# Kernel optimization log

Hardware: AMD Instinct MI355X
Metric: run time of the kernel (lower is better)

## Reference

```python
import jax, jax.numpy as jnp
import numpy as np

N_NODES = 100000
N_EDGES = 1600000
IN_C, HID_C, OUT_C = 128, 128, 64


def gcn_conv(x, src, dst, n_nodes, W, b):
    # PyG GCNConv (normalize=True, add_self_loops=True):
    # out = D^{-1/2} (A+I) D^{-1/2} (x @ W^T) + b
    h = x @ W.T                                   # [N, out]
    deg = jax.ops.segment_sum(jnp.ones(src.shape, x.dtype), dst,
                              num_segments=n_nodes)  # includes self-loops
    dinv = jnp.where(deg > 0, jax.lax.rsqrt(deg), 0.0)
    norm = dinv[src] * dinv[dst]                  # [E+N]
    msg = h[src] * norm[:, None]                  # gather + scale
    out = jax.ops.segment_sum(msg, dst, num_segments=n_nodes)
    return out + b


def setup_inputs() -> dict:
    key = jax.random.key(0)
    ks = jax.random.split(key, 8)
    x = jax.random.normal(ks[0], (N_NODES, IN_C), dtype=jnp.float32)
    edge_index = jax.random.randint(ks[1], (2, N_EDGES), 0, N_NODES, dtype=jnp.int64)

    def lin(k, fan_out, fan_in):
        s = 1.0 / np.sqrt(fan_in)
        kw, kb = jax.random.split(k)
        W = jax.random.uniform(kw, (fan_out, fan_in), jnp.float32, -s, s)
        b = jax.random.uniform(kb, (fan_out,), jnp.float32, -s, s)
        return W, b

    W1, b1 = lin(ks[2], HID_C, IN_C)
    W2, b2 = lin(ks[3], HID_C, HID_C)
    W3, b3 = lin(ks[4], OUT_C, HID_C)
    return {"x": x, "edge_index": edge_index,
            "W1": W1, "b1": b1, "W2": W2, "b2": b2, "W3": W3, "b3": b3}


def reference(x, edge_index, W1, b1, W2, b2, W3, b3):
    n = x.shape[0]
    loop = jnp.arange(n, dtype=edge_index.dtype)
    src = jnp.concatenate([edge_index[0], loop])  # add self-loops once; identical per layer
    dst = jnp.concatenate([edge_index[1], loop])
    h = gcn_conv(x, src, dst, n, W1, b1)
    h = jax.nn.relu(h)
    h = gcn_conv(h, src, dst, n, W2, b2)
    h = jax.nn.relu(h)
    h = gcn_conv(h, src, dst, n, W3, b3)
    return h
```

## Files before the change

### kernel.cpp

```cpp
#include <hip/hip_runtime.h>


#define NPB 256
#define CAP 4672
#define BIN_WGS 128

typedef short bfrag __attribute__((ext_vector_type(8)));
typedef float f32x4 __attribute__((ext_vector_type(4)));
typedef unsigned short u16x8 __attribute__((ext_vector_type(8)));

__global__ __launch_bounds__(256) void init_cur(int* __restrict__ cur, int B) {
  int i = blockIdx.x * 256 + threadIdx.x;
  if (i < B) cur[i] = i * CAP;
}

__global__ __launch_bounds__(256) void bin_edges(const int* __restrict__ src,
                                                 const int* __restrict__ dst,
                                                 int* __restrict__ cur,
                                                 int* __restrict__ binned,
                                                 int E, int B) {
  __shared__ int lc[512];
  __shared__ int lbase[512];
  const int t = threadIdx.x;
  const int chunk = (E + BIN_WGS - 1) / BIN_WGS;
  const int e0 = blockIdx.x * chunk;
  const int e1 = min(E, e0 + chunk);

  for (int i = t; i < B; i += 256) lc[i] = 0;
  __syncthreads();
  for (int e = e0 + t; e < e1; e += 256) {
    int d = dst[e];
    atomicAdd(&lc[d >> 8], 1);
  }
  __syncthreads();
  for (int i = t; i < B; i += 256) {
    int c = lc[i];
    lbase[i] = c ? atomicAdd(&cur[i], c) : 0;
    lc[i] = 0;
  }
  __syncthreads();
  for (int e = e0 + t; e < e1; e += 256) {
    int d = dst[e];
    int s = __builtin_nontemporal_load(&src[e]);
    int bk = d >> 8;
    int p = lbase[bk] + atomicAdd(&lc[bk], 1);
    if (p < (bk + 1) * CAP)
      binned[p] = ((d & 255) << 24) | s;
  }
}

__global__ __launch_bounds__(256) void build_buckets(const int* __restrict__ binned,
                                                     const int* __restrict__ cur,
                                                     int* __restrict__ cols,
                                                     int2* __restrict__ off2,
                                                     float* __restrict__ dinv,
                                                     int N) {
  __shared__ int eb[CAP];
  __shared__ int ob[CAP];
  __shared__ int lc[256];
  __shared__ int sc[256];
  const int b = blockIdx.x;
  const int t = threadIdx.x;
  const int base = b * CAP;
  const int cntb = min(cur[b] - base, CAP);

  for (int i = t; i < cntb; i += 256) eb[i] = binned[base + i];
  lc[t] = 0;
  __syncthreads();
  for (int i = t; i < cntb; i += 256)
    atomicAdd(&lc[(unsigned)eb[i] >> 24], 1);
  __syncthreads();
  int myc = lc[t];
  sc[t] = myc;
  __syncthreads();
  for (int d = 1; d < 256; d <<= 1) {
    int a = (t >= d) ? sc[t - d] : 0;
    __syncthreads();
    sc[t] += a;
    __syncthreads();
  }
  int excl = sc[t] - myc;
  int node = b * NPB + t;
  if (node < N) {
    off2[node] = make_int2(base + excl, base + excl + myc);
    dinv[node] = rsqrtf((float)(myc + 1));
  }
  lc[t] = excl;
  __syncthreads();
  for (int i = t; i < cntb; i += 256) {
    int e = eb[i];
    int p = atomicAdd(&lc[(unsigned)e >> 24], 1);
    ob[p] = e & 0xFFFFFF;
  }
  __syncthreads();
  for (int i = t; i < cntb; i += 256) cols[base + i] = ob[i];
}

__device__ inline unsigned short bf16rne(float x) {
  unsigned u = __float_as_uint(x);
  return (unsigned short)((u + 0x7FFFu + ((u >> 16) & 1u)) >> 16);
}
__device__ inline float bf16lo(unsigned q) { return __uint_as_float(q << 16); }
__device__ inline float bf16hi(unsigned q) { return __uint_as_float(q & 0xFFFF0000u); }

#define LDP 136
template <int OUTC>
__global__ __launch_bounds__(256) void gemm_xw_mfma(const float* __restrict__ X,
                                                    const float* __restrict__ W,
                                                    const float* __restrict__ dinv,
                                                    unsigned short* __restrict__ Y,
                                                    int M) {
  __shared__ unsigned short Xhi[64 * LDP], Xlo[64 * LDP];
  __shared__ unsigned short Whi[64 * LDP], Wlo[64 * LDP];
  const int tid = threadIdx.x;
  const int m_base = blockIdx.x * 64;

  for (int idx = tid; idx < 64 * 16; idx += 256) {
    int r = idx >> 4, g = idx & 15;
    int m = m_base + r;
    float4 v0 = make_float4(0.f, 0.f, 0.f, 0.f), v1 = v0;
    if (m < M) {
      const float4* px = (const float4*)(X + (size_t)m * 128 + g * 8);
      v0 = px[0];
      v1 = px[1];
    }
    float vv[8] = {v0.x, v0.y, v0.z, v0.w, v1.x, v1.y, v1.z, v1.w};
    u16x8 hv, lv;
#pragma unroll
    for (int j = 0; j < 8; ++j) {
      unsigned short h = bf16rne(vv[j]);
      float res = vv[j] - __uint_as_float((unsigned)h << 16);
      hv[j] = h;
      lv[j] = bf16rne(res);
    }
    *(u16x8*)(Xhi + r * LDP + g * 8) = hv;
    *(u16x8*)(Xlo + r * LDP + g * 8) = lv;
  }

  const int lane = tid & 63;
  const int wv = tid >> 6;
  const int col_l = lane & 15;
  const int quad = lane >> 4;
  const int aBase = (wv * 16 + col_l) * LDP + quad * 8;
  const int bBase = col_l * LDP + quad * 8;

  for (int cc = 0; cc < OUTC; cc += 64) {
    __syncthreads();
    for (int idx = tid; idx < 64 * 16; idx += 256) {
      int r = idx >> 4, g = idx & 15;
      const float4* pw = (const float4*)(W + (size_t)(cc + r) * 128 + g * 8);
      float4 v0 = pw[0], v1 = pw[1];
      float vv[8] = {v0.x, v0.y, v0.z, v0.w, v1.x, v1.y, v1.z, v1.w};
      u16x8 hv, lv;
#pragma unroll
      for (int j = 0; j < 8; ++j) {
        unsigned short h = bf16rne(vv[j]);
        float res = vv[j] - __uint_as_float((unsigned)h << 16);
        hv[j] = h;
        lv[j] = bf16rne(res);
      }
      *(u16x8*)(Whi + r * LDP + g * 8) = hv;
      *(u16x8*)(Wlo + r * LDP + g * 8) = lv;
    }
    __syncthreads();

    f32x4 acc[4] = {{0.f, 0.f, 0.f, 0.f},
                    {0.f, 0.f, 0.f, 0.f},
                    {0.f, 0.f, 0.f, 0.f},
                    {0.f, 0.f, 0.f, 0.f}};
#pragma unroll
    for (int ks = 0; ks < 4; ++ks) {
      int ao = aBase + ks * 32;
      bfrag aHi = *(const bfrag*)(Xhi + ao);
      bfrag aLo = *(const bfrag*)(Xlo + ao);
#pragma unroll
      for (int t = 0; t < 4; ++t) {
        int bo = bBase + t * 16 * LDP + ks * 32;
        bfrag bHi = *(const bfrag*)(Whi + bo);
        bfrag bLo = *(const bfrag*)(Wlo + bo);
        acc[t] = __builtin_amdgcn_mfma_f32_16x16x32_bf16(aHi, bHi, acc[t], 0, 0, 0);
        acc[t] = __builtin_amdgcn_mfma_f32_16x16x32_bf16(aLo, bHi, acc[t], 0, 0, 0);
        acc[t] = __builtin_amdgcn_mfma_f32_16x16x32_bf16(aHi, bLo, acc[t], 0, 0, 0);
      }
    }

#pragma unroll
    for (int r = 0; r < 4; ++r) {
      int row = m_base + wv * 16 + quad * 4 + r;
      if (row < M) {
        float s = dinv[row];
#pragma unroll
        for (int t = 0; t < 4; ++t) {
          unsigned short h = bf16rne(acc[t][r] * s);
          Y[(size_t)row * OUTC + cc + t * 16 + col_l] = h;
        }
      }
    }
  }
}

template <int C, bool RELU>
__global__ __launch_bounds__(256) void aggregate(const void* __restrict__ xsv,
                                                 const int2* __restrict__ off2,
                                                 const int* __restrict__ cols,
                                                 const float* __restrict__ dinv,
                                                 const float* __restrict__ bias,
                                                 float* __restrict__ out, int N) {
  constexpr int V = C / 64;
  int wid = (int)((blockIdx.x * blockDim.x + threadIdx.x) >> 6);
  int lane = threadIdx.x & 63;
  if (wid >= N) return;

  float a0, a1 = 0.f;
  if constexpr (V == 2) {
    const unsigned* xs = (const unsigned*)xsv;
    unsigned q = xs[(size_t)wid * 64 + lane];
    a0 = bf16lo(q);
    a1 = bf16hi(q);
  } else {
    const unsigned short* xs = (const unsigned short*)xsv;
    a0 = __uint_as_float((unsigned)xs[(size_t)wid * 64 + lane] << 16);
  }

  int2 oo = off2[wid];
  int ebase = oo.x;
  int e1 = oo.y;
  while (ebase < e1) {
    int cnt = e1 - ebase;
    if (cnt > 64) cnt = 64;
    int col = (lane < cnt) ? __builtin_nontemporal_load(&cols[ebase + lane]) : 0;
    int j = 0;
    for (; j + 4 <= cnt; j += 4) {
      int s0 = __shfl(col, j), s1 = __shfl(col, j + 1);
      int s2 = __shfl(col, j + 2), s3 = __shfl(col, j + 3);
      if constexpr (V == 2) {
        const unsigned* xs = (const unsigned*)xsv;
        unsigned q0 = xs[(size_t)s0 * 64 + lane];
        unsigned q1 = xs[(size_t)s1 * 64 + lane];
        unsigned q2 = xs[(size_t)s2 * 64 + lane];
        unsigned q3 = xs[(size_t)s3 * 64 + lane];
        a0 += (bf16lo(q0) + bf16lo(q1)) + (bf16lo(q2) + bf16lo(q3));
        a1 += (bf16hi(q0) + bf16hi(q1)) + (bf16hi(q2) + bf16hi(q3));
      } else {
        const unsigned short* xs = (const unsigned short*)xsv;
        float t0 = __uint_as_float((unsigned)xs[(size_t)s0 * 64 + lane] << 16);
        float t1 = __uint_as_float((unsigned)xs[(size_t)s1 * 64 + lane] << 16);
        float t2 = __uint_as_float((unsigned)xs[(size_t)s2 * 64 + lane] << 16);
        float t3 = __uint_as_float((unsigned)xs[(size_t)s3 * 64 + lane] << 16);
        a0 += (t0 + t1) + (t2 + t3);
      }
    }
    for (; j < cnt; ++j) {
      int s = __shfl(col, j);
      if constexpr (V == 2) {
        const unsigned* xs = (const unsigned*)xsv;
        unsigned q = xs[(size_t)s * 64 + lane];
        a0 += bf16lo(q);
        a1 += bf16hi(q);
      } else {
        const unsigned short* xs = (const unsigned short*)xsv;
        a0 += __uint_as_float((unsigned)xs[(size_t)s * 64 + lane] << 16);
      }
    }
    ebase += cnt;
  }

  float dd = dinv[wid];
  if constexpr (V == 2) {
    float o0 = a0 * dd + bias[lane * 2];
    float o1 = a1 * dd + bias[lane * 2 + 1];
    if (RELU) {
      o0 = fmaxf(o0, 0.f);
      o1 = fmaxf(o1, 0.f);
    }
    __builtin_nontemporal_store(o0, &out[(size_t)wid * C + lane * 2]);
    __builtin_nontemporal_store(o1, &out[(size_t)wid * C + lane * 2 + 1]);
  } else {
    float o0 = a0 * dd + bias[lane];
    if (RELU) o0 = fmaxf(o0, 0.f);
    __builtin_nontemporal_store(o0, &out[(size_t)wid * C + lane]);
  }
}


extern "C" void kernel_launch(void* const* d_in, const int* in_sizes, int n_in,
                              void* d_out, int out_size, void* d_ws, size_t ws_size,
                              hipStream_t stream) {
  const float* x  = (const float*)d_in[0];
  const int*   ei = (const int*)d_in[1];
  const float* W1 = (const float*)d_in[2];
  const float* b1 = (const float*)d_in[3];
  const float* W2 = (const float*)d_in[4];
  const float* b2 = (const float*)d_in[5];
  const float* W3 = (const float*)d_in[6];
  const float* b3 = (const float*)d_in[7];

  const int N = in_sizes[0] / 128;
  const int E = in_sizes[1] / 2;
  const int* src = ei;
  const int* dst = ei + E;
  const int B = (N + NPB - 1) / NPB;

  char* w = (char*)d_ws;
  size_t p = 0;
  auto alloc = [&](size_t bytes) -> void* {
    void* r = w + p;
    p = (p + bytes + 255) & ~(size_t)255;
    return r;
  };
  float*    dinv   = (float*)alloc((size_t)N * 4);
  int2*     off2   = (int2*)alloc((size_t)N * 8);
  int*      cur    = (int*)alloc((size_t)B * 4);
  int*      binned = (int*)alloc((size_t)B * CAP * 4);
  int*      cols   = (int*)alloc((size_t)B * CAP * 4);
  unsigned short* xsb = (unsigned short*)alloc((size_t)N * 128 * 2);
  float*    bufB   = (float*)alloc((size_t)N * 128 * 4);

  init_cur<<<(B + 255) / 256, 256, 0, stream>>>(cur, B);
  bin_edges<<<BIN_WGS, 256, 0, stream>>>(src, dst, cur, binned, E, B);
  build_buckets<<<B, 256, 0, stream>>>(binned, cur, cols, off2, dinv, N);

  const int gb = (N + 63) / 64;
  const int ab = (N + 3) / 4;

  gemm_xw_mfma<128><<<gb, 256, 0, stream>>>(x, W1, dinv, xsb, N);
  aggregate<128, true><<<ab, 256, 0, stream>>>(xsb, off2, cols, dinv, b1, bufB, N);
  gemm_xw_mfma<128><<<gb, 256, 0, stream>>>(bufB, W2, dinv, xsb, N);
  aggregate<128, true><<<ab, 256, 0, stream>>>(xsb, off2, cols, dinv, b2, bufB, N);
  gemm_xw_mfma<64><<<gb, 256, 0, stream>>>(bufB, W3, dinv, xsb, N);
  aggregate<64, false><<<ab, 256, 0, stream>>>(xsb, off2, cols, dinv, b3,
                                               (float*)d_out, N);
}
```

Measured before the change: 459.5 us.

## Use 16-byte gathers over multiple edges per wave in aggregation; presplit weights

The aggregation kernel now has each lane load 8 bf16 channels (16 bytes) per neighbor, so a 64-lane wave covers several edges at once. Partial sums are then reduced across edge groups with xor-shuffles, and the output is written as vector stores. This targets the many small 4-byte gathers and the serial per-edge loop of the old kernel, at the cost of a cross-lane reduction and some masked wasted loads. Separately, the weight hi/lo bf16 split moves into a small pre-kernel, so each GEMM block no longer recomputes it.

```diff
diff --git a/kernel.cpp b/kernel.cpp
--- a/kernel.cpp
+++ b/kernel.cpp
@@ -103,10 +103,24 @@
 __device__ inline float bf16lo(unsigned q) { return __uint_as_float(q << 16); }
 __device__ inline float bf16hi(unsigned q) { return __uint_as_float(q & 0xFFFF0000u); }
 
+__global__ __launch_bounds__(256) void split_w(const float* __restrict__ W,
+                                               unsigned short* __restrict__ hi,
+                                               unsigned short* __restrict__ lo,
+                                               int total) {
+  int i = blockIdx.x * 256 + threadIdx.x;
+  if (i < total) {
+    float v = W[i];
+    unsigned short h = bf16rne(v);
+    hi[i] = h;
+    lo[i] = bf16rne(v - __uint_as_float((unsigned)h << 16));
+  }
+}
+
 #define LDP 136
 template <int OUTC>
 __global__ __launch_bounds__(256) void gemm_xw_mfma(const float* __restrict__ X,
-                                                    const float* __restrict__ W,
+                                                    const unsigned short* __restrict__ Whg,
+                                                    const unsigned short* __restrict__ Wlg,
                                                     const float* __restrict__ dinv,
                                                     unsigned short* __restrict__ Y,
                                                     int M) {
@@ -148,17 +162,8 @@
     __syncthreads();
     for (int idx = tid; idx < 64 * 16; idx += 256) {
       int r = idx >> 4, g = idx & 15;
-      const float4* pw = (const float4*)(W + (size_t)(cc + r) * 128 + g * 8);
-      float4 v0 = pw[0], v1 = pw[1];
-      float vv[8] = {v0.x, v0.y, v0.z, v0.w, v1.x, v1.y, v1.z, v1.w};
-      u16x8 hv, lv;
-#pragma unroll
-      for (int j = 0; j < 8; ++j) {
-        unsigned short h = bf16rne(vv[j]);
-        float res = vv[j] - __uint_as_float((unsigned)h << 16);
-        hv[j] = h;
-        lv[j] = bf16rne(res);
-      }
+      u16x8 hv = *(const u16x8*)(Whg + (size_t)(cc + r) * 128 + g * 8);
+      u16x8 lv = *(const u16x8*)(Wlg + (size_t)(cc + r) * 128 + g * 8);
       *(u16x8*)(Whi + r * LDP + g * 8) = hv;
       *(u16x8*)(Wlo + r * LDP + g * 8) = lv;
     }
@@ -200,85 +205,99 @@
 }
 
 template <int C, bool RELU>
-__global__ __launch_bounds__(256) void aggregate(const void* __restrict__ xsv,
-                                                 const int2* __restrict__ off2,
-                                                 const int* __restrict__ cols,
-                                                 const float* __restrict__ dinv,
-                                                 const float* __restrict__ bias,
-                                                 float* __restrict__ out, int N) {
-  constexpr int V = C / 64;
+__global__ __launch_bounds__(256) void aggregate2(const unsigned short* __restrict__ xs,
+                                                  const int2* __restrict__ off2,
+                                                  const int* __restrict__ cols,
+                                                  const float* __restrict__ dinv,
+                                                  const float* __restrict__ bias,
+                                                  float* __restrict__ out, int N) {
+  constexpr int CG = C / 8;
+  constexpr int EG = 64 / CG;
   int wid = (int)((blockIdx.x * blockDim.x + threadIdx.x) >> 6);
   int lane = threadIdx.x & 63;
   if (wid >= N) return;
-
-  float a0, a1 = 0.f;
-  if constexpr (V == 2) {
-    const unsigned* xs = (const unsigned*)xsv;
-    unsigned q = xs[(size_t)wid * 64 + lane];
-    a0 = bf16lo(q);
-    a1 = bf16hi(q);
-  } else {
-    const unsigned short* xs = (const unsigned short*)xsv;
-    a0 = __uint_as_float((unsigned)xs[(size_t)wid * 64 + lane] << 16);
+  const int eg = lane / CG;
+  const int cg = lane % CG;
+
+  float acc[8] = {0.f, 0.f, 0.f, 0.f, 0.f, 0.f, 0.f, 0.f};
+  if (eg == 0) {
+    uint4 d = *(const uint4*)(xs + (size_t)wid * C + cg * 8);
+    acc[0] = bf16lo(d.x); acc[1] = bf16hi(d.x);
+    acc[2] = bf16lo(d.y); acc[3] = bf16hi(d.y);
+    acc[4] = bf16lo(d.z); acc[5] = bf16hi(d.z);
+    acc[6] = bf16lo(d.w); acc[7] = bf16hi(d.w);
   }
 
   int2 oo = off2[wid];
   int ebase = oo.x;
-  int e1 = oo.y;
-  while (ebase < e1) {
-    int cnt = e1 - ebase;
+  const int eend = oo.y;
+  while (ebase < eend) {
+    int cnt = eend - ebase;
     if (cnt > 64) cnt = 64;
     int col = (lane < cnt) ? __builtin_nontemporal_load(&cols[ebase + lane]) : 0;
-    int j = 0;
-    for (; j + 4 <= cnt; j += 4) {
-      int s0 = __shfl(col, j), s1 = __shfl(col, j + 1);
-      int s2 = __shfl(col, j + 2), s3 = __shfl(col, j + 3);
-      if constexpr (V == 2) {
-        const unsigned* xs = (const unsigned*)xsv;
-        unsigned q0 = xs[(size_t)s0 * 64 + lane];
-        unsigned q1 = xs[(size_t)s1 * 64 + lane];
-        unsigned q2 = xs[(size_t)s2 * 64 + lane];
-        unsigned q3 = xs[(size_t)s3 * 64 + lane];
-        a0 += (bf16lo(q0) + bf16lo(q1)) + (bf16lo(q2) + bf16lo(q3));
-        a1 += (bf16hi(q0) + bf16hi(q1)) + (bf16hi(q2) + bf16hi(q3));
-      } else {
-        const unsigned short* xs = (const unsigned short*)xsv;
-        float t0 = __uint_as_float((unsigned)xs[(size_t)s0 * 64 + lane] << 16);
-        float t1 = __uint_as_float((unsigned)xs[(size_t)s1 * 64 + lane] << 16);
-        float t2 = __uint_as_float((unsigned)xs[(size_t)s2 * 64 + lane] << 16);
-        float t3 = __uint_as_float((unsigned)xs[(size_t)s3 * 64 + lane] << 16);
-        a0 += (t0 + t1) + (t2 + t3);
-      }
-    }
-    for (; j < cnt; ++j) {
-      int s = __shfl(col, j);
-      if constexpr (V == 2) {
-        const unsigned* xs = (const unsigned*)xsv;
-        unsigned q = xs[(size_t)s * 64 + lane];
-        a0 += bf16lo(q);
-        a1 += bf16hi(q);
-      } else {
-        const unsigned short* xs = (const unsigned short*)xsv;
-        a0 += __uint_as_float((unsigned)xs[(size_t)s * 64 + lane] << 16);
+    const int c1 = cnt - 1;
+    for (int j = 0; j < cnt; j += 4 * EG) {
+      int i0 = j + eg, i1 = i0 + EG, i2 = i1 + EG, i3 = i2 + EG;
+      int s0 = __shfl(col, min(i0, c1));
+      int s1 = __shfl(col, min(i1, c1));
+      int s2 = __shfl(col, min(i2, c1));
+      int s3 = __shfl(col, min(i3, c1));
+      uint4 d0 = *(const uint4*)(xs + (size_t)s0 * C + cg * 8);
+      uint4 d1 = *(const uint4*)(xs + (size_t)s1 * C + cg * 8);
+      uint4 d2 = *(const uint4*)(xs + (size_t)s2 * C + cg * 8);
+      uint4 d3 = *(const uint4*)(xs + (size_t)s3 * C + cg * 8);
+      if (i0 < cnt) {
+        acc[0] += bf16lo(d0.x); acc[1] += bf16hi(d0.x);
+        acc[2] += bf16lo(d0.y); acc[3] += bf16hi(d0.y);
+        acc[4] += bf16lo(d0.z); acc[5] += bf16hi(d0.z);
+        acc[6] += bf16lo(d0.w); acc[7] += bf16hi(d0.w);
+      }
+      if (i1 < cnt) {
+        acc[0] += bf16lo(d1.x); acc[1] += bf16hi(d1.x);
+        acc[2] += bf16lo(d1.y); acc[3] += bf16hi(d1.y);
+        acc[4] += bf16lo(d1.z); acc[5] += bf16hi(d1.z);
+        acc[6] += bf16lo(d1.w); acc[7] += bf16hi(d1.w);
+      }
+      if (i2 < cnt) {
+        acc[0] += bf16lo(d2.x); acc[1] += bf16hi(d2.x);
+        acc[2] += bf16lo(d2.y); acc[3] += bf16hi(d2.y);
+        acc[4] += bf16lo(d2.z); acc[5] += bf16hi(d2.z);
+        acc[6] += bf16lo(d2.w); acc[7] += bf16hi(d2.w);
+      }
+      if (i3 < cnt) {
+        acc[0] += bf16lo(d3.x); acc[1] += bf16hi(d3.x);
+        acc[2] += bf16lo(d3.y); acc[3] += bf16hi(d3.y);
+        acc[4] += bf16lo(d3.z); acc[5] += bf16hi(d3.z);
+        acc[6] += bf16lo(d3.w); acc[7] += bf16hi(d3.w);
       }
     }
     ebase += cnt;
   }
 
-  float dd = dinv[wid];
-  if constexpr (V == 2) {
-    float o0 = a0 * dd + bias[lane * 2];
-    float o1 = a1 * dd + bias[lane * 2 + 1];
+#pragma unroll
+  for (int m = CG; m < 64; m <<= 1) {
+#pragma unroll
+    for (int q = 0; q < 8; ++q) acc[q] += __shfl_xor(acc[q], m);
+  }
+
+  if (eg == 0) {
+    float dd = dinv[wid];
+    const float4 bA = *(const float4*)(bias + cg * 8);
+    const float4 bB = *(const float4*)(bias + cg * 8 + 4);
+    f32x4 oA, oB;
+    oA[0] = acc[0] * dd + bA.x; oA[1] = acc[1] * dd + bA.y;
+    oA[2] = acc[2] * dd + bA.z; oA[3] = acc[3] * dd + bA.w;
+    oB[0] = acc[4] * dd + bB.x; oB[1] = acc[5] * dd + bB.y;
+    oB[2] = acc[6] * dd + bB.z; oB[3] = acc[7] * dd + bB.w;
     if (RELU) {
-      o0 = fmaxf(o0, 0.f);
-      o1 = fmaxf(o1, 0.f);
-    }
-    __builtin_nontemporal_store(o0, &out[(size_t)wid * C + lane * 2]);
-    __builtin_nontemporal_store(o1, &out[(size_t)wid * C + lane * 2 + 1]);
-  } else {
-    float o0 = a0 * dd + bias[lane];
-    if (RELU) o0 = fmaxf(o0, 0.f);
-    __builtin_nontemporal_store(o0, &out[(size_t)wid * C + lane]);
+#pragma unroll
+      for (int q = 0; q < 4; ++q) {
+        oA[q] = fmaxf(oA[q], 0.f);
+        oB[q] = fmaxf(oB[q], 0.f);
+      }
+    }
+    __builtin_nontemporal_store(oA, (f32x4*)(out + (size_t)wid * C + cg * 8));
+    __builtin_nontemporal_store(oB, (f32x4*)(out + (size_t)wid * C + cg * 8 + 4));
   }
 }
 
@@ -315,19 +334,28 @@
   int*      cols   = (int*)alloc((size_t)B * CAP * 4);
   unsigned short* xsb = (unsigned short*)alloc((size_t)N * 128 * 2);
   float*    bufB   = (float*)alloc((size_t)N * 128 * 4);
+  unsigned short* w1h = (unsigned short*)alloc(128 * 128 * 2);
+  unsigned short* w1l = (unsigned short*)alloc(128 * 128 * 2);
+  unsigned short* w2h = (unsigned short*)alloc(128 * 128 * 2);
+  unsigned short* w2l = (unsigned short*)alloc(128 * 128 * 2);
+  unsigned short* w3h = (unsigned short*)alloc(64 * 128 * 2);
+  unsigned short* w3l = (unsigned short*)alloc(64 * 128 * 2);
 
   init_cur<<<(B + 255) / 256, 256, 0, stream>>>(cur, B);
   bin_edges<<<BIN_WGS, 256, 0, stream>>>(src, dst, cur, binned, E, B);
+  split_w<<<64, 256, 0, stream>>>(W1, w1h, w1l, 128 * 128);
+  split_w<<<64, 256, 0, stream>>>(W2, w2h, w2l, 128 * 128);
+  split_w<<<32, 256, 0, stream>>>(W3, w3h, w3l, 64 * 128);
   build_buckets<<<B, 256, 0, stream>>>(binned, cur, cols, off2, dinv, N);
 
   const int gb = (N + 63) / 64;
   const int ab = (N + 3) / 4;
 
-  gemm_xw_mfma<128><<<gb, 256, 0, stream>>>(x, W1, dinv, xsb, N);
-  aggregate<128, true><<<ab, 256, 0, stream>>>(xsb, off2, cols, dinv, b1, bufB, N);
-  gemm_xw_mfma<128><<<gb, 256, 0, stream>>>(bufB, W2, dinv, xsb, N);
-  aggregate<128, true><<<ab, 256, 0, stream>>>(xsb, off2, cols, dinv, b2, bufB, N);
-  gemm_xw_mfma<64><<<gb, 256, 0, stream>>>(bufB, W3, dinv, xsb, N);
-  aggregate<64, false><<<ab, 256, 0, stream>>>(xsb, off2, cols, dinv, b3,
-                                               (float*)d_out, N);
-}
+  gemm_xw_mfma<128><<<gb, 256, 0, stream>>>(x, w1h, w1l, dinv, xsb, N);
+  aggregate2<128, true><<<ab, 256, 0, stream>>>(xsb, off2, cols, dinv, b1, bufB, N);
+  gemm_xw_mfma<128><<<gb, 256, 0, stream>>>(bufB, w2h, w2l, dinv, xsb, N);
+  aggregate2<128, true><<<ab, 256, 0, stream>>>(xsb, off2, cols, dinv, b2, bufB, N);
+  gemm_xw_mfma<64><<<gb, 256, 0, stream>>>(bufB, w3h, w3l, dinv, xsb, N);
+  aggregate2<64, false><<<ab, 256, 0, stream>>>(xsb, off2, cols, dinv, b3,
+                                                (float*)d_out, N);
+}
```

After: 443.6 us. 1.04x faster.
